# Kernel tuning notes

Measured on AMD Instinct MI355X. Metric: run time of the kernel, lower is better.

Reference implementation:

```python
import jax, jax.numpy as jnp
import numpy as np

CP = 1.0   # polynomial kernel balance (Kerv2d cp)
DP = 2     # polynomial kernel degree (Kerv2d dp)
EPS = 1e-5 # BatchNorm eps


def kerv2d(x, w, stride, padding):
    # polynomial kervolution: (patch . w + cp) ** dp, computed as conv then pointwise
    y = jax.lax.conv_general_dilated(
        x, w,
        window_strides=(stride, stride),
        padding=[(padding, padding), (padding, padding)],
        dimension_numbers=('NCHW', 'OIHW', 'NCHW'))
    return (y + CP) ** DP


def bn(x, g, b, m, v):
    # inference-mode BatchNorm2d with running stats, folded to scale/shift
    inv = g / jnp.sqrt(v + EPS)
    return x * inv[None, :, None, None] + (b - m * inv)[None, :, None, None]


def setup_inputs() -> dict:
    key = jax.random.key(0)
    ks = jax.random.split(key, 4)
    C_in, C_mid = 1024, 256  # bottleneck: 1024 -> 256 -> 256 -> 1024
    d = {
        'x':  jax.random.normal(ks[0], (128, C_in, 14, 14), jnp.float32),
        'w1': jax.random.normal(ks[1], (C_mid, C_in, 1, 1), jnp.float32) * 0.03,
        'w2': jax.random.normal(ks[2], (C_mid, C_mid, 3, 3), jnp.float32) * 0.02,
        'w3': jax.random.normal(ks[3], (C_in, C_mid, 1, 1), jnp.float32) * 0.03,
    }
    for i, c in zip((1, 2, 3), (C_mid, C_mid, C_in)):
        d[f'g{i}'] = jnp.ones((c,), jnp.float32)
        d[f'b{i}'] = jnp.zeros((c,), jnp.float32)
        d[f'm{i}'] = jnp.zeros((c,), jnp.float32)
        d[f'v{i}'] = jnp.ones((c,), jnp.float32)
    return d


def reference(x, w1, w2, w3, g1, b1, m1, v1, g2, b2, m2, v2, g3, b3, m3, v3):
    identity = x
    h = bn(kerv2d(x, w1, 1, 0), g1, b1, m1, v1)   # 1x1 kerv + BN (num_layers>34 branch)
    h = bn(kerv2d(h, w2, 1, 1), g2, b2, m2, v2)   # 3x3 kerv + BN, stride=1
    h = bn(kerv2d(h, w3, 1, 0), g3, b3, m3, v3)   # 1x1 kerv (expansion=4) + BN
    return h + identity                           # residual add (identity_downsample=None)
```

## Files before the change

kernel.cpp:

```cpp
#include <hip/hip_runtime.h>

using f32x4 = __attribute__((ext_vector_type(4))) float;
using s16x8 = __attribute__((ext_vector_type(8))) short;
using s16x4 = __attribute__((ext_vector_type(4))) short;

#define P_PIX 196
#define NPIX_ALL (128 * 196)
#define NROW  208
#define NR2   104
#define KT    32

static __device__ __forceinline__ short f2bf(float f) {
  union { float f; unsigned u; } a; a.f = f;
  unsigned u = a.u;
  u += 0x7fffu + ((u >> 16) & 1u);
  return (short)(u >> 16);
}

static __device__ __forceinline__ f32x4 mfma16(s16x8 a, s16x8 b, f32x4 c) {
  return __builtin_amdgcn_mfma_f32_16x16x32_bf16(a, b, c, 0, 0, 0);
}

static __device__ __forceinline__ void gload16(const short* g, short* l) {
  __builtin_amdgcn_global_load_lds(
      (const __attribute__((address_space(1))) unsigned int*)(g),
      (__attribute__((address_space(3))) unsigned int*)(l), 16, 0, 0);
}

static __device__ __forceinline__ const s16x8* fragp(const short* buf, int row, int l4) {
  return (const s16x8*)(buf + row * KT + ((l4 ^ ((row >> 1) & 3)) << 3));
}

static __device__ __forceinline__ void stage(const short* __restrict__ src, int srcK,
                                             int k0, short* dst, int rows, int rmax,
                                             int tid) {
  for (int t = tid; t < rows * 4; t += 256) {
    int r = t >> 2, c = t & 3;
    int rr = r < rmax ? r : rmax;
    int cs = c ^ ((r >> 1) & 3);
    gload16(src + (size_t)rr * srcK + k0 + cs * 8, dst + t * 8);
  }
}


__global__ void k_prep(const float* __restrict__ w1, const float* __restrict__ w2,
                       const float* __restrict__ w3,
                       const float* g1, const float* b1, const float* m1, const float* v1,
                       const float* g2, const float* b2, const float* m2, const float* v2,
                       const float* g3, const float* b3, const float* m3, const float* v3,
                       float* bn, short* W1b, short* W2t, short* W3b) {
  int i = blockIdx.x * 256 + threadIdx.x;
  if (i < 65536) {
    f32x4 v = *(const f32x4*)(w1 + i * 4);
    s16x4 o;
    o[0] = f2bf(v[0]); o[1] = f2bf(v[1]); o[2] = f2bf(v[2]); o[3] = f2bf(v[3]);
    *(s16x4*)(W1b + i * 4) = o;
  } else if (i < 131072) {
    int q = i - 65536;
    f32x4 v = *(const f32x4*)(w3 + q * 4);
    s16x4 o;
    o[0] = f2bf(v[0]); o[1] = f2bf(v[1]); o[2] = f2bf(v[2]); o[3] = f2bf(v[3]);
    *(s16x4*)(W3b + q * 4) = o;
  } else if (i < 278528) {
    int q = (i - 131072) * 4;
    s16x4 o;
    #pragma unroll
    for (int k = 0; k < 4; ++k) {
      int idx = q + k;
      int s = idx >> 16, rem = idx & 65535;
      int co = rem >> 8, ci = rem & 255;
      o[k] = f2bf(w2[(co * 256 + ci) * 9 + s]);
    }
    *(s16x4*)(W2t + q) = o;
  } else if (i < 280064) {
    int t = i - 278528;
    if (t < 256) {
      float inv = g1[t] * rsqrtf(v1[t] + 1e-5f);
      bn[t] = inv; bn[256 + t] = b1[t] - m1[t] * inv;
    } else if (t < 512) {
      int c = t - 256;
      float inv = g2[c] * rsqrtf(v2[c] + 1e-5f);
      bn[512 + c] = inv; bn[768 + c] = b2[c] - m2[c] * inv;
    } else {
      int c = t - 512;
      float inv = g3[c] * rsqrtf(v3[c] + 1e-5f);
      bn[1024 + c] = inv; bn[2048 + c] = b3[c] - m3[c] * inv;
    }
  }
}


__global__ __launch_bounds__(256) void k_layer1(
    const float* __restrict__ x, const short* __restrict__ W1b,
    const float* __restrict__ bnbuf, short* __restrict__ H1) {
  __shared__ __align__(16) short lB[2][128 * KT];
  const int tid = threadIdx.x;
  const int b = blockIdx.x;
  const int n = b >> 2, mb = (b >> 1) & 1, jh = b & 1;
  const int lane = tid & 63, wave = tid >> 6;
  const int l15 = lane & 15, l4 = lane >> 4;

  if (jh == 1 && tid < 96) {
    int bb = tid / 48, idx = tid % 48;
    s16x8 z = {0,0,0,0,0,0,0,0};
    *(s16x8*)(&lB[bb][100 * KT + idx * 8]) = z;
  }

  const float* xs = x + (size_t)n * 1024 * P_PIX;
  const short* Asrc = W1b + (size_t)(mb * 128) * 1024;

  const int npg = jh ? 25 : 28;
  const int pgbase = jh ? 24 : 0;
  const bool act = tid < npg * 8;
  const int pg = pgbase + (act ? tid % npg : 0);
  const int kg = act ? tid / npg : 0;
  const int lrow0 = pg * 4 - jh * 96;

  f32x4 rX[4], rY[4];
  auto loadx = [&](int kt, f32x4* r) {
    if (!act) return;
    const float* sp = xs + (size_t)(kt * 32 + kg * 4) * P_PIX + pg * 4;
    r[0] = *(const f32x4*)sp;
    r[1] = *(const f32x4*)(sp + P_PIX);
    r[2] = *(const f32x4*)(sp + 2 * P_PIX);
    r[3] = *(const f32x4*)(sp + 3 * P_PIX);
  };
  auto cvtw = [&](const f32x4* r, short* buf) {
    if (!act) return;
    int chunk = kg >> 1, inner = (kg & 1) * 4;
    #pragma unroll
    for (int q = 0; q < 4; ++q) {
      int lr = lrow0 + q;
      s16x4 w;
      w[0] = f2bf(r[0][q]); w[1] = f2bf(r[1][q]);
      w[2] = f2bf(r[2][q]); w[3] = f2bf(r[3][q]);
      *(s16x4*)(buf + lr * KT + ((chunk ^ ((lr >> 1) & 3)) << 3) + inner) = w;
    }
  };

  f32x4 acc[2][7];
  f32x4 zero = {0.f, 0.f, 0.f, 0.f};
  #pragma unroll
  for (int m = 0; m < 2; ++m)
    #pragma unroll
    for (int jj = 0; jj < 7; ++jj) acc[m][jj] = zero;

  loadx(0, rX);
  loadx(1, rY);
  cvtw(rX, lB[0]);
  __syncthreads();

  auto body = [&](int kt, f32x4* rNext, f32x4* rFill) {
    if (kt + 2 < 32) loadx(kt + 2, rFill);
    s16x8 a0 = *(const s16x8*)(Asrc + (size_t)(wave * 32 + l15) * 1024 + kt * 32 + l4 * 8);
    s16x8 a1 = *(const s16x8*)(Asrc + (size_t)(wave * 32 + 16 + l15) * 1024 + kt * 32 + l4 * 8);
    const short* B = lB[kt & 1];
    #pragma unroll
    for (int jj = 0; jj < 7; ++jj) {
      s16x8 bfr = *fragp(B, jj * 16 + l15, l4);
      acc[0][jj] = mfma16(a0, bfr, acc[0][jj]);
      acc[1][jj] = mfma16(a1, bfr, acc[1][jj]);
    }
    if (kt + 1 < 32) cvtw(rNext, lB[(kt + 1) & 1]);
    __syncthreads();
  };

  for (int kt = 0; kt < 32; kt += 2) {
    body(kt, rY, rX);
    body(kt + 1, rX, rY);
  }

  short* Hn = H1 + (size_t)n * P_PIX * 256;
  #pragma unroll
  for (int m = 0; m < 2; ++m) {
    int co = mb * 128 + wave * 32 + m * 16 + l4 * 4;
    f32x4 sc = *(const f32x4*)(bnbuf + co);
    f32x4 sh = *(const f32x4*)(bnbuf + 256 + co);
    #pragma unroll
    for (int jj = 0; jj < 7; ++jj) {
      if (jh && jj == 0) continue;
      int p = (jh * 6 + jj) * 16 + l15;
      if (p < P_PIX) {
        s16x4 o;
        #pragma unroll
        for (int i = 0; i < 4; ++i) {
          float y = acc[m][jj][i] + 1.0f;
          o[i] = f2bf(y * y * sc[i] + sh[i]);
        }
        *(s16x4*)(Hn + p * 256 + co) = o;
      }
    }
  }
}


__global__ __launch_bounds__(256) void k_layer2(
    const short* __restrict__ H1, const short* __restrict__ W2t,
    const float* __restrict__ bnbuf, short* __restrict__ H2) {
  __shared__ __align__(16) short lB[2][NROW * KT];
  const int tid = threadIdx.x;
  const int b = blockIdx.x;
  const int n = b >> 2, mb = (b >> 1) & 1, jh = b & 1;
  const int lane = tid & 63, wave = tid >> 6;
  const int l15 = lane & 15, l4 = lane >> 4;

  if (tid < 8) {
    int bb = tid >> 2, idx = tid & 3;
    s16x8 z = {0,0,0,0,0,0,0,0};
    *(s16x8*)(&lB[bb][196 * KT + idx * 8]) = z;
  }

  int vm[7];
  #pragma unroll
  for (int jj = 0; jj < 7; ++jj) {
    int p = (jh * 6 + jj) * 16 + l15;
    int m = 0;
    if (p < P_PIX) {
      int h = p / 14, w = p % 14;
      m = 2 | 16;
      if (h >= 1)  m |= 1;
      if (h < 13)  m |= 4;
      if (w >= 1)  m |= 8;
      if (w < 13)  m |= 32;
    }
    vm[jj] = m;
  }

  f32x4 acc[2][7];
  f32x4 zero = {0.f, 0.f, 0.f, 0.f};
  #pragma unroll
  for (int m = 0; m < 2; ++m)
    #pragma unroll
    for (int jj = 0; jj < 7; ++jj) acc[m][jj] = zero;

  const short* Bsrc = H1 + (size_t)n * P_PIX * 256;

  stage(Bsrc, 256, 0, lB[0], P_PIX, P_PIX - 1, tid);
  __syncthreads();

  for (int kt = 0; kt < 8; ++kt) {
    if (kt < 7)
      stage(Bsrc, 256, (kt + 1) * 32, lB[(kt + 1) & 1], P_PIX, P_PIX - 1, tid);
    const short* B = lB[kt & 1];
    #pragma unroll
    for (int s = 0; s < 9; ++s) {
      const int dy = s / 3, dx = s % 3;
      const int doff = (dy - 1) * 14 + (dx - 1);
      const size_t arow = (size_t)(s * 256 + mb * 128 + wave * 32 + l15) * 256 + kt * 32 + l4 * 8;
      s16x8 a0 = *(const s16x8*)(W2t + arow);
      s16x8 a1 = *(const s16x8*)(W2t + arow + 16 * 256);
      #pragma unroll
      for (int jj = 0; jj < 7; ++jj) {
        int p = (jh * 6 + jj) * 16 + l15;
        bool valid = ((vm[jj] >> dy) & 1) && ((vm[jj] >> (3 + dx)) & 1);
        int row = valid ? (p + doff) : 196;
        s16x8 bfr = *fragp(B, row, l4);
        acc[0][jj] = mfma16(a0, bfr, acc[0][jj]);
        acc[1][jj] = mfma16(a1, bfr, acc[1][jj]);
      }
    }
    __syncthreads();
  }

  short* Hn = H2 + (size_t)n * P_PIX * 256;
  #pragma unroll
  for (int m = 0; m < 2; ++m) {
    int co = mb * 128 + wave * 32 + m * 16 + l4 * 4;
    f32x4 sc = *(const f32x4*)(bnbuf + 512 + co);
    f32x4 sh = *(const f32x4*)(bnbuf + 768 + co);
    #pragma unroll
    for (int jj = 0; jj < 7; ++jj) {
      if (jh && jj == 0) continue;
      int p = (jh * 6 + jj) * 16 + l15;
      if (p < P_PIX) {
        s16x4 o;
        #pragma unroll
        for (int i = 0; i < 4; ++i) {
          float y = acc[m][jj][i] + 1.0f;
          o[i] = f2bf(y * y * sc[i] + sh[i]);
        }
        *(s16x4*)(Hn + p * 256 + co) = o;
      }
    }
  }
}


__global__ __launch_bounds__(256) void k_layer3(
    const short* __restrict__ H2, const short* __restrict__ W3b,
    const float* __restrict__ bnbuf, const float* __restrict__ x,
    float* __restrict__ out) {
  __shared__ __align__(16) char smem[14336];
  short* const lB0 = (short*)smem;
  short* const lB1 = lB0 + 112 * KT;
  float* const eb = (float*)smem;

  const int tid = threadIdx.x;
  const int tile = blockIdx.x >> 4, mb = blockIdx.x & 15;
  const int lane = tid & 63, wave = tid >> 6;
  const int l15 = lane & 15, l4 = lane >> 4;
  const int P0 = tile * NR2;
  const int rmax = NPIX_ALL - 1 - P0;

  const short* Asrc = W3b + (size_t)(mb * 64) * 256;
  const short* Bsrc = H2 + (size_t)P0 * 256;

  f32x4 acc[7];
  f32x4 zero = {0.f, 0.f, 0.f, 0.f};
  #pragma unroll
  for (int j = 0; j < 7; ++j) acc[j] = zero;

  stage(Bsrc, 256, 0, lB0, NR2, rmax, tid);
  __syncthreads();

  for (int kt = 0; kt < 8; ++kt) {
    if (kt < 7)
      stage(Bsrc, 256, (kt + 1) * 32, ((kt + 1) & 1) ? lB1 : lB0, NR2, rmax, tid);
    s16x8 a = *(const s16x8*)(Asrc + (size_t)(wave * 16 + l15) * 256 + kt * 32 + l4 * 8);
    const short* B = (kt & 1) ? lB1 : lB0;
    #pragma unroll
    for (int j = 0; j < 7; ++j) {
      s16x8 bfr = *fragp(B, j * 16 + l15, l4);
      acc[j] = mfma16(a, bfr, acc[j]);
    }
    __syncthreads();
  }

  const int co_r = tid >> 3;
  const int pcb  = tid & 7;
  #pragma unroll
  for (int h = 0; h < 2; ++h) {
    __syncthreads();
    if ((wave >> 1) == h) {
      const int co_l = (wave & 1) * 16 + l4 * 4;
      #pragma unroll
      for (int j = 0; j < 7; ++j) {
        const int p = j * 16 + l15;
        #pragma unroll
        for (int i = 0; i < 4; ++i)
          eb[(co_l + i) * 112 + p] = acc[j][i];
      }
    }
    __syncthreads();
    const int co_g = mb * 64 + h * 32 + co_r;
    const float scv = bnbuf[1024 + co_g];
    const float shv = bnbuf[2048 + co_g];
    #pragma unroll
    for (int pass = 0; pass < 4; ++pass) {
      const int pc = pcb + pass * 8;
      if (pc < 26) {
        const int P = P0 + pc * 4;
        if (P < NPIX_ALL) {
          f32x4 v = *(const f32x4*)(eb + co_r * 112 + pc * 4);
          const int nn = P / P_PIX, pp = P - nn * P_PIX;
          const size_t idx = ((size_t)(nn * 1024 + co_g)) * P_PIX + pp;
          f32x4 xv = *(const f32x4*)(x + idx);
          f32x4 o;
          #pragma unroll
          for (int k = 0; k < 4; ++k) {
            float y = v[k] + 1.0f;
            o[k] = y * y * scv + shv + xv[k];
          }
          *(f32x4*)(out + idx) = o;
        }
      }
    }
  }
}


extern "C" void kernel_launch(void* const* d_in, const int* in_sizes, int n_in,
                              void* d_out, int out_size, void* d_ws, size_t ws_size,
                              hipStream_t stream) {
  (void)in_sizes; (void)n_in; (void)out_size; (void)ws_size;
  const float* x  = (const float*)d_in[0];
  const float* w1 = (const float*)d_in[1];
  const float* w2 = (const float*)d_in[2];
  const float* w3 = (const float*)d_in[3];
  const float* g1 = (const float*)d_in[4];
  const float* b1 = (const float*)d_in[5];
  const float* m1 = (const float*)d_in[6];
  const float* v1 = (const float*)d_in[7];
  const float* g2 = (const float*)d_in[8];
  const float* b2 = (const float*)d_in[9];
  const float* m2 = (const float*)d_in[10];
  const float* v2 = (const float*)d_in[11];
  const float* g3 = (const float*)d_in[12];
  const float* b3 = (const float*)d_in[13];
  const float* m3 = (const float*)d_in[14];
  const float* v3 = (const float*)d_in[15];

  char* ws = (char*)d_ws;
  short* W1b   = (short*)(ws + 0);
  short* W2t   = (short*)(ws + 524288);
  short* W3b   = (short*)(ws + 1703936);
  float* bnbuf = (float*)(ws + 2228224);
  short* H1    = (short*)(ws + 2240512);
  short* H2    = (short*)(ws + 15085568);

  k_prep<<<1094, 256, 0, stream>>>(w1, w2, w3,
                                   g1, b1, m1, v1, g2, b2, m2, v2, g3, b3, m3, v3,
                                   bnbuf, W1b, W2t, W3b);
  k_layer1<<<512, 256, 0, stream>>>(x, W1b, bnbuf, H1);
  k_layer2<<<512, 256, 0, stream>>>(H1, W2t, bnbuf, H2);
  k_layer3<<<3872, 256, 0, stream>>>(H2, W3b, bnbuf, x, (float*)d_out);
}
```

Baseline: 157.3 us.

## Remap block indices across XCDs and retile layer2/layer3 work decomposition

Block indices in all three layer kernels are permuted so consecutive virtual blocks land on the same XCD (blockIdx & 7 chooses the group), which should improve L2 locality for blocks sharing the same image or weights. Layer2 now splits each image's pixels into quarters instead of halves, doubling the grid to 1024 blocks with fewer accumulators per thread. Layer3 now processes one whole image (208 padded rows) per block instead of 104-pixel tiles. That removes the cross-image index arithmetic and the boundary checks, at the cost of more LDS and more accumulators per thread. Layer2 blocks now restage the full image per quarter, so H1 traffic through the caches rises.

```diff
diff --git a/kernel.cpp b/kernel.cpp
--- a/kernel.cpp
+++ b/kernel.cpp
@@ -7,7 +7,6 @@
 #define P_PIX 196
 #define NPIX_ALL (128 * 196)
 #define NROW  208
-#define NR2   104
 #define KT    32
 
 static __device__ __forceinline__ short f2bf(float f) {
@@ -95,8 +94,8 @@
     const float* __restrict__ bnbuf, short* __restrict__ H1) {
   __shared__ __align__(16) short lB[2][128 * KT];
   const int tid = threadIdx.x;
-  const int b = blockIdx.x;
-  const int n = b >> 2, mb = (b >> 1) & 1, jh = b & 1;
+  const int vb = (blockIdx.x & 7) * 64 + (blockIdx.x >> 3);
+  const int n = vb >> 2, mb = (vb >> 1) & 1, jh = vb & 1;
   const int lane = tid & 63, wave = tid >> 6;
   const int l15 = lane & 15, l4 = lane >> 4;
 
@@ -199,8 +198,8 @@
     const float* __restrict__ bnbuf, short* __restrict__ H2) {
   __shared__ __align__(16) short lB[2][NROW * KT];
   const int tid = threadIdx.x;
-  const int b = blockIdx.x;
-  const int n = b >> 2, mb = (b >> 1) & 1, jh = b & 1;
+  const int vb = (blockIdx.x & 7) * 128 + (blockIdx.x >> 3);
+  const int n = vb >> 3, mb = (vb >> 2) & 1, jq = vb & 3;
   const int lane = tid & 63, wave = tid >> 6;
   const int l15 = lane & 15, l4 = lane >> 4;
 
@@ -210,10 +209,10 @@
     *(s16x8*)(&lB[bb][196 * KT + idx * 8]) = z;
   }
 
-  int vm[7];
-  #pragma unroll
-  for (int jj = 0; jj < 7; ++jj) {
-    int p = (jh * 6 + jj) * 16 + l15;
+  int vm[4];
+  #pragma unroll
+  for (int jj = 0; jj < 4; ++jj) {
+    int p = (jq * 3 + jj) * 16 + l15;
     int m = 0;
     if (p < P_PIX) {
       int h = p / 14, w = p % 14;
@@ -226,12 +225,12 @@
     vm[jj] = m;
   }
 
-  f32x4 acc[2][7];
+  f32x4 acc[2][4];
   f32x4 zero = {0.f, 0.f, 0.f, 0.f};
   #pragma unroll
   for (int m = 0; m < 2; ++m)
     #pragma unroll
-    for (int jj = 0; jj < 7; ++jj) acc[m][jj] = zero;
+    for (int jj = 0; jj < 4; ++jj) acc[m][jj] = zero;
 
   const short* Bsrc = H1 + (size_t)n * P_PIX * 256;
 
@@ -250,8 +249,8 @@
       s16x8 a0 = *(const s16x8*)(W2t + arow);
       s16x8 a1 = *(const s16x8*)(W2t + arow + 16 * 256);
       #pragma unroll
-      for (int jj = 0; jj < 7; ++jj) {
-        int p = (jh * 6 + jj) * 16 + l15;
+      for (int jj = 0; jj < 4; ++jj) {
+        int p = (jq * 3 + jj) * 16 + l15;
         bool valid = ((vm[jj] >> dy) & 1) && ((vm[jj] >> (3 + dx)) & 1);
         int row = valid ? (p + doff) : 196;
         s16x8 bfr = *fragp(B, row, l4);
@@ -269,9 +268,9 @@
     f32x4 sc = *(const f32x4*)(bnbuf + 512 + co);
     f32x4 sh = *(const f32x4*)(bnbuf + 768 + co);
     #pragma unroll
-    for (int jj = 0; jj < 7; ++jj) {
-      if (jh && jj == 0) continue;
-      int p = (jh * 6 + jj) * 16 + l15;
+    for (int jj = 0; jj < 4; ++jj) {
+      if (jq && jj == 0) continue;
+      int p = (jq * 3 + jj) * 16 + l15;
       if (p < P_PIX) {
         s16x4 o;
         #pragma unroll
@@ -290,36 +289,35 @@
     const short* __restrict__ H2, const short* __restrict__ W3b,
     const float* __restrict__ bnbuf, const float* __restrict__ x,
     float* __restrict__ out) {
-  __shared__ __align__(16) char smem[14336];
+  __shared__ __align__(16) char smem[27136];
   short* const lB0 = (short*)smem;
-  short* const lB1 = lB0 + 112 * KT;
+  short* const lB1 = lB0 + NROW * KT;
   float* const eb = (float*)smem;
 
   const int tid = threadIdx.x;
-  const int tile = blockIdx.x >> 4, mb = blockIdx.x & 15;
+  const int vb = (blockIdx.x & 7) * 256 + (blockIdx.x >> 3);
+  const int n = vb >> 4, mb = vb & 15;
   const int lane = tid & 63, wave = tid >> 6;
   const int l15 = lane & 15, l4 = lane >> 4;
-  const int P0 = tile * NR2;
-  const int rmax = NPIX_ALL - 1 - P0;
 
   const short* Asrc = W3b + (size_t)(mb * 64) * 256;
-  const short* Bsrc = H2 + (size_t)P0 * 256;
-
-  f32x4 acc[7];
+  const short* Bsrc = H2 + (size_t)n * P_PIX * 256;
+
+  f32x4 acc[13];
   f32x4 zero = {0.f, 0.f, 0.f, 0.f};
   #pragma unroll
-  for (int j = 0; j < 7; ++j) acc[j] = zero;
-
-  stage(Bsrc, 256, 0, lB0, NR2, rmax, tid);
+  for (int j = 0; j < 13; ++j) acc[j] = zero;
+
+  stage(Bsrc, 256, 0, lB0, NROW, P_PIX - 1, tid);
   __syncthreads();
 
   for (int kt = 0; kt < 8; ++kt) {
     if (kt < 7)
-      stage(Bsrc, 256, (kt + 1) * 32, ((kt + 1) & 1) ? lB1 : lB0, NR2, rmax, tid);
+      stage(Bsrc, 256, (kt + 1) * 32, ((kt + 1) & 1) ? lB1 : lB0, NROW, P_PIX - 1, tid);
     s16x8 a = *(const s16x8*)(Asrc + (size_t)(wave * 16 + l15) * 256 + kt * 32 + l4 * 8);
     const short* B = (kt & 1) ? lB1 : lB0;
     #pragma unroll
-    for (int j = 0; j < 7; ++j) {
+    for (int j = 0; j < 13; ++j) {
       s16x8 bfr = *fragp(B, j * 16 + l15, l4);
       acc[j] = mfma16(a, bfr, acc[j]);
     }
@@ -334,35 +332,32 @@
     if ((wave >> 1) == h) {
       const int co_l = (wave & 1) * 16 + l4 * 4;
       #pragma unroll
-      for (int j = 0; j < 7; ++j) {
+      for (int j = 0; j < 13; ++j) {
         const int p = j * 16 + l15;
         #pragma unroll
         for (int i = 0; i < 4; ++i)
-          eb[(co_l + i) * 112 + p] = acc[j][i];
+          eb[(co_l + i) * 212 + p] = acc[j][i];
       }
     }
     __syncthreads();
     const int co_g = mb * 64 + h * 32 + co_r;
     const float scv = bnbuf[1024 + co_g];
     const float shv = bnbuf[2048 + co_g];
-    #pragma unroll
-    for (int pass = 0; pass < 4; ++pass) {
+    const size_t rowbase = ((size_t)(n * 1024 + co_g)) * P_PIX;
+    #pragma unroll
+    for (int pass = 0; pass < 7; ++pass) {
       const int pc = pcb + pass * 8;
-      if (pc < 26) {
-        const int P = P0 + pc * 4;
-        if (P < NPIX_ALL) {
-          f32x4 v = *(const f32x4*)(eb + co_r * 112 + pc * 4);
-          const int nn = P / P_PIX, pp = P - nn * P_PIX;
-          const size_t idx = ((size_t)(nn * 1024 + co_g)) * P_PIX + pp;
-          f32x4 xv = *(const f32x4*)(x + idx);
-          f32x4 o;
-          #pragma unroll
-          for (int k = 0; k < 4; ++k) {
-            float y = v[k] + 1.0f;
-            o[k] = y * y * scv + shv + xv[k];
-          }
-          *(f32x4*)(out + idx) = o;
+      if (pc < 49) {
+        f32x4 v = *(const f32x4*)(eb + co_r * 212 + pc * 4);
+        const size_t idx = rowbase + pc * 4;
+        f32x4 xv = *(const f32x4*)(x + idx);
+        f32x4 o;
+        #pragma unroll
+        for (int k = 0; k < 4; ++k) {
+          float y = v[k] + 1.0f;
+          o[k] = y * y * scv + shv + xv[k];
         }
+        *(f32x4*)(out + idx) = o;
       }
     }
   }
@@ -402,6 +397,6 @@
                                    g1, b1, m1, v1, g2, b2, m2, v2, g3, b3, m3, v3,
                                    bnbuf, W1b, W2t, W3b);
   k_layer1<<<512, 256, 0, stream>>>(x, W1b, bnbuf, H1);
-  k_layer2<<<512, 256, 0, stream>>>(H1, W2t, bnbuf, H2);
-  k_layer3<<<3872, 256, 0, stream>>>(H2, W3b, bnbuf, x, (float*)d_out);
-}
+  k_layer2<<<1024, 256, 0, stream>>>(H1, W2t, bnbuf, H2);
+  k_layer3<<<2048, 256, 0, stream>>>(H2, W3b, bnbuf, x, (float*)d_out);
+}
```

Measured after the change: 171.5 us. 9.0% more time.
